# Performance work log

Measured on AMD Instinct MI355X. Metric: run time of the kernel, lower is better.

The kernel has to match this reference:

```python
import jax, jax.numpy as jnp
import numpy as np

EPS = 1e-8
LN_EPS = 1e-5
MA_K = 25


def _moving_avg(x, k):
    # x: [B, L]; replicate-pad by (k-1)//2 on each side, then length-k mean -> [B, L]
    p = (k - 1) // 2
    xp = jnp.concatenate([jnp.repeat(x[:, :1], p, axis=1), x, jnp.repeat(x[:, -1:], p, axis=1)], axis=1)
    cs = jnp.concatenate([jnp.zeros((x.shape[0], 1), x.dtype), jnp.cumsum(xp, axis=1)], axis=1)
    return (cs[:, k:] - cs[:, :-k]) / k


def _acf(xc, den, lag):
    # xc: mean-centered x [B, L]; den: sum(xc^2)+eps [B]
    num = (xc[:, :-lag] * xc[:, lag:]).sum(axis=1)
    return jnp.clip(num / den, -1.0, 1.0)


def _forward(x, ln_w, ln_b, w1, b1, w2, b2):
    B, L = x.shape
    trend = _moving_avg(x, MA_K)
    resid = x - trend

    m = x.mean(axis=1, keepdims=True)
    xc = x - m
    den = (xc * xc).sum(axis=1) + EPS

    acf1 = _acf(xc, den, 1)
    acf2 = _acf(xc, den, 2)

    # spectral entropy + peak psd ratio (single rfft)
    Xf = jnp.fft.rfft(x, axis=1)
    psd = jnp.maximum(Xf.real ** 2 + Xf.imag ** 2, EPS)
    psd_sum = psd.sum(axis=1)
    psd_n = psd / psd_sum[:, None]
    ent = -(psd_n * jnp.log(psd_n + EPS)).sum(axis=1)
    max_ent = jnp.log(jnp.asarray(psd.shape[1], x.dtype) + EPS)
    spent = jnp.clip(ent / (max_ent + EPS), 0.0, 1.0)
    peak_ratio = jnp.clip(psd.max(axis=1) / (psd_sum + EPS), 0.0, 1.0)

    # unit-root phi
    x_t, x_tm1 = x[:, 1:], x[:, :-1]
    phi = jnp.clip((x_t * x_tm1).sum(axis=1) / ((x_tm1 ** 2).sum(axis=1) + EPS), -1.0, 1.0)

    diff = x_t - x_tm1
    diff_var = jnp.var(diff, axis=1)
    trend_strength = jnp.var(trend, axis=1)
    kpss_proxy = jnp.var(jnp.cumsum(resid, axis=1), axis=1) / (jnp.var(x, axis=1) + 1e-8)

    h = max(1, min(10, L // 4))
    lbq = sum(_acf(xc, den, k) ** 2 for k in range(1, h + 1))

    feats = jnp.stack([acf1, acf2, spent, phi, diff_var, trend_strength, kpss_proxy, lbq, peak_ratio], axis=1)

    # LayerNorm over 9 features
    fm = feats.mean(axis=-1, keepdims=True)
    fv = jnp.var(feats, axis=-1, keepdims=True)
    feats_n = (feats - fm) / jnp.sqrt(fv + LN_EPS) * ln_w + ln_b

    # MLP router: 9 -> 64 -> 3 (dropout=0, temperature=1)
    hdd = jax.nn.relu(feats_n @ w1 + b1)
    logits = hdd @ w2 + b2
    weights = jax.nn.softmax(logits, axis=-1)
    return weights, feats_n


def setup_inputs() -> dict:
    key = jax.random.key(0)
    ks = jax.random.split(key, 5)
    B, L, D, H, C = 32768, 1024, 9, 64, 3
    return {
        "x_n_target": jax.random.normal(ks[0], (B, L), dtype=jnp.float32),
        "ln_w": jnp.ones((D,), jnp.float32),
        "ln_b": jnp.zeros((D,), jnp.float32),
        "w1": jax.random.normal(ks[1], (D, H), dtype=jnp.float32) * 0.3,
        "b1": jnp.zeros((H,), jnp.float32),
        "w2": jax.random.normal(ks[2], (H, C), dtype=jnp.float32) * 0.1,
        "b2": jnp.zeros((C,), jnp.float32),
    }


def reference(x_n_target, ln_w, ln_b, w1, b1, w2, b2):
    return _forward(x_n_target, ln_w, ln_b, w1, b1, w2, b2)
```

## Files before the change

kernel.cpp:

```cpp
#include <hip/hip_runtime.h>
#include <math.h>

#define EPSF 1e-8f

typedef float f2v __attribute__((ext_vector_type(2)));

__device__ __forceinline__ float bcf(int x){ return __builtin_bit_cast(float, x); }
__device__ __forceinline__ int   bci(float x){ return __builtin_bit_cast(int, x); }

template<int CTRL, int RM>
__device__ __forceinline__ float dpp0(float v){
  return bcf(__builtin_amdgcn_update_dpp(0, bci(v), CTRL, RM, 0xF, false));
}
__device__ __forceinline__ float rl(float v, int l){
  return bcf(__builtin_amdgcn_readlane(bci(v), l));
}
__device__ __forceinline__ float wave_iscan_add(float v){
  v += dpp0<0x111,0xF>(v);
  v += dpp0<0x112,0xF>(v);
  v += dpp0<0x114,0xF>(v);
  v += dpp0<0x118,0xF>(v);
  v += dpp0<0x142,0xA>(v);
  v += dpp0<0x143,0xC>(v);
  return v;
}
__device__ __forceinline__ float wave_red_add(float v){ return wave_iscan_add(v); }
__device__ __forceinline__ float wave_red_max_pos(float v){
  v = fmaxf(v, dpp0<0x111,0xF>(v));
  v = fmaxf(v, dpp0<0x112,0xF>(v));
  v = fmaxf(v, dpp0<0x114,0xF>(v));
  v = fmaxf(v, dpp0<0x118,0xF>(v));
  v = fmaxf(v, dpp0<0x142,0xA>(v));
  v = fmaxf(v, dpp0<0x143,0xC>(v));
  return v;
}

__device__ __forceinline__ int FL8(int i){ return i ^ ((i >> 3) & 7); }

__device__ __forceinline__ void dft8p(f2v* ar, f2v* ai){
  const float C = 0.70710678118654752f;
  const f2v t0r=ar[0]+ar[4], t0i=ai[0]+ai[4];
  const f2v t1r=ar[0]-ar[4], t1i=ai[0]-ai[4];
  const f2v t2r=ar[2]+ar[6], t2i=ai[2]+ai[6];
  const f2v t3r=ar[2]-ar[6], t3i=ai[2]-ai[6];
  const f2v E0r=t0r+t2r, E0i=t0i+t2i;
  const f2v E1r=t1r+t3i, E1i=t1i-t3r;
  const f2v E2r=t0r-t2r, E2i=t0i-t2i;
  const f2v E3r=t1r-t3i, E3i=t1i+t3r;
  const f2v u0r=ar[1]+ar[5], u0i=ai[1]+ai[5];
  const f2v u1r=ar[1]-ar[5], u1i=ai[1]-ai[5];
  const f2v u2r=ar[3]+ar[7], u2i=ai[3]+ai[7];
  const f2v u3r=ar[3]-ar[7], u3i=ai[3]-ai[7];
  const f2v O0r=u0r+u2r, O0i=u0i+u2i;
  const f2v O1r=u1r+u3i, O1i=u1i-u3r;
  const f2v O2r=u0r-u2r, O2i=u0i-u2i;
  const f2v O3r=u1r-u3i, O3i=u1i+u3r;
  const f2v w1r =  C*(O1r+O1i), w1i = C*(O1i-O1r);
  const f2v w2r =  O2i,         w2i = -O2r;
  const f2v w3r =  C*(O3i-O3r), w3i = -C*(O3r+O3i);
  ar[0]=E0r+O0r; ai[0]=E0i+O0i;
  ar[4]=E0r-O0r; ai[4]=E0i-O0i;
  ar[1]=E1r+w1r; ai[1]=E1i+w1i;
  ar[5]=E1r-w1r; ai[5]=E1i-w1i;
  ar[2]=E2r+w2r; ai[2]=E2i+w2i;
  ar[6]=E2r-w2r; ai[6]=E2i-w2i;
  ar[3]=E3r+w3r; ai[3]=E3i+w3i;
  ar[7]=E3r-w3r; ai[7]=E3i-w3i;
}

__global__ void __launch_bounds__(128, 2)
sr_kernel(const float* __restrict__ x,
          const float* __restrict__ ln_w, const float* __restrict__ ln_b,
          const float* __restrict__ w1, const float* __restrict__ b1,
          const float* __restrict__ w2, const float* __restrict__ b2,
          float* __restrict__ out, int B)
{
  __shared__ __align__(16) float bufr2[2][2048];
  __shared__ __align__(16) float stats2[2][2][40];

  const int tid = threadIdx.x;
  const int t   = tid & 63;
  const int wv  = tid >> 6;
  const int rowbase = blockIdx.x * 4 + wv * 2;
  if (rowbase >= B) return;
  float* buff = bufr2[wv];

#pragma unroll 1
  for (int rr = 0; rr < 2; ++rr) {
    const float* __restrict__ xr = x + (size_t)(rowbase + rr) * 1024;
    float* st = stats2[wv][rr];

    const int c0 = t * 16;
    float vv[28];
    {
      const float4 a0 = *reinterpret_cast<const float4*>(xr + c0);
      const float4 a1 = *reinterpret_cast<const float4*>(xr + c0 + 4);
      const float4 a2 = *reinterpret_cast<const float4*>(xr + c0 + 8);
      const float4 a3 = *reinterpret_cast<const float4*>(xr + c0 + 12);
      vv[0]=a0.x; vv[1]=a0.y; vv[2]=a0.z; vv[3]=a0.w;
      vv[4]=a1.x; vv[5]=a1.y; vv[6]=a1.z; vv[7]=a1.w;
      vv[8]=a2.x; vv[9]=a2.y; vv[10]=a2.z; vv[11]=a2.w;
      vv[12]=a3.x; vv[13]=a3.y; vv[14]=a3.z; vv[15]=a3.w;
      if (t < 63) {
        const float4 n0 = *reinterpret_cast<const float4*>(xr + c0 + 16);
        const float4 n1 = *reinterpret_cast<const float4*>(xr + c0 + 20);
        const float4 n2 = *reinterpret_cast<const float4*>(xr + c0 + 24);
        vv[16]=n0.x; vv[17]=n0.y; vv[18]=n0.z; vv[19]=n0.w;
        vv[20]=n1.x; vv[21]=n1.y; vv[22]=n1.z; vv[23]=n1.w;
        vv[24]=n2.x; vv[25]=n2.y; vv[26]=n2.z; vv[27]=n2.w;
      } else {
#pragma unroll
        for (int j = 16; j < 28; ++j) vv[j] = 0.f;
      }
    }
    float pv[12];
    if (t > 0) {
      const float4 p0 = *reinterpret_cast<const float4*>(xr + c0 - 12);
      const float4 p1 = *reinterpret_cast<const float4*>(xr + c0 - 8);
      const float4 p2 = *reinterpret_cast<const float4*>(xr + c0 - 4);
      pv[0]=p0.x; pv[1]=p0.y; pv[2]=p0.z; pv[3]=p0.w;
      pv[4]=p1.x; pv[5]=p1.y; pv[6]=p1.z; pv[7]=p1.w;
      pv[8]=p2.x; pv[9]=p2.y; pv[10]=p2.z; pv[11]=p2.w;
    } else {
#pragma unroll
      for (int j = 0; j < 12; ++j) pv[j] = 0.f;
    }

#pragma unroll
    for (int j = 0; j < 8; ++j) {
      const int fo = FL8(8*t + j) * 4 + rr;
      buff[fo]     = vv[2*j];
      buff[fo + 2] = vv[2*j + 1];
    }

    {
      float sumsq = 0.f, alt = 0.f;
#pragma unroll
      for (int j = 0; j < 16; ++j) {
        sumsq = fmaf(vv[j], vv[j], sumsq);
        alt += (j & 1) ? -vv[j] : vv[j];
      }
      float r;
      r = wave_red_add(sumsq); if (t == 63) st[0] = r;
      r = wave_red_add(alt);   if (t == 63) st[1] = r;
    }
#pragma unroll
    for (int k = 1; k <= 10; ++k) {
      float acc = 0.f;
#pragma unroll
      for (int j = 0; j < 16; ++j) acc = fmaf(vv[j], vv[j+k], acc);
      float r = wave_red_add(acc);
      if (t == 63) st[1 + k] = r;
    }

    float s[16];
    s[0] = vv[0];
#pragma unroll
    for (int j = 1; j < 16; ++j) s[j] = s[j-1] + vv[j];
    const float cs16 = s[15];
    const float incl = wave_iscan_add(cs16);
    const float excl = incl - cs16;
#pragma unroll
    for (int j = 0; j < 16; ++j) s[j] += excl;
    if (t == 63) st[16] = incl;
    if (t == 0) {
#pragma unroll
      for (int q = 0; q < 10; ++q) st[17 + q] = s[q];
      st[37] = vv[0];
    }
    if (t == 63) {
#pragma unroll
      for (int q = 0; q < 10; ++q) st[27 + q] = s[5 + q];
      st[38] = vv[15];
    }

    float trv[16];
    float str = 0.f, str2 = 0.f;
    {
      float wsum = 0.f;
#pragma unroll
      for (int j = 0; j < 12; ++j) wsum += pv[j];
#pragma unroll
      for (int j = 0; j <= 12; ++j) wsum += vv[j];
#pragma unroll
      for (int jj = 0; jj < 16; ++jj) {
        if (jj > 0) {
          const float addv = vv[jj + 12];
          const float subv = (jj < 13) ? pv[jj - 1] : vv[jj - 13];
          wsum += addv - subv;
        }
        float swc = wsum;
        if (t == 0  && jj < 12) swc += (float)(12 - jj) * vv[0];
        if (t == 63 && jj >= 4) swc += (float)(jj - 3) * vv[15];
        const float tv = swc * 0.04f;
        trv[jj] = tv;
        str += tv;
        str2 = fmaf(tv, tv, str2);
      }
    }
    const float tincl = wave_iscan_add(str);
    if (t == 63) st[12] = tincl;
    { float r = wave_red_add(str2); if (t == 63) st[13] = r; }
    {
      const float texcl = tincl - str;
      float run = texcl, sc = 0.f, sc2 = 0.f;
#pragma unroll
      for (int jj = 0; jj < 16; ++jj) {
        run += trv[jj];
        const float cv = s[jj] - run;
        sc += cv;
        sc2 = fmaf(cv, cv, sc2);
      }
      float r;
      r = wave_red_add(sc);  if (t == 63) st[14] = r;
      r = wave_red_add(sc2); if (t == 63) st[15] = r;
    }
  }

  f2v zr[8], zi[8];
#pragma unroll
  for (int p = 0; p < 8; ++p) {
    const float4 q4 = *reinterpret_cast<const float4*>(&buff[FL8(t + 64*p) * 4]);
    zr[p] = f2v{q4.x, q4.y};
    zi[p] = f2v{q4.z, q4.w};
  }
  dft8p(zr, zi);
  {
    const float a1 = -0.012271846303085130f * (float)t;
    const float c1 = __cosf(a1), s1 = __sinf(a1);
    const float c2=c1*c1-s1*s1, s2=2.f*c1*s1;
    const float c3=c2*c1-s2*s1, s3=s2*c1+c2*s1;
    const float c4=c2*c2-s2*s2, s4=2.f*c2*s2;
    const float c5=c4*c1-s4*s1, s5=s4*c1+c4*s1;
    const float c6=c3*c3-s3*s3, s6=2.f*c3*s3;
    const float c7=c6*c1-s6*s1, s7=s6*c1+c6*s1;
    const float cq[8] = {1.f,c1,c2,c3,c4,c5,c6,c7};
    const float sq[8] = {0.f,s1,s2,s3,s4,s5,s6,s7};
#pragma unroll
    for (int q = 1; q < 8; ++q) {
      const f2v r0 = zr[q]*cq[q] - zi[q]*sq[q];
      zi[q] = zr[q]*sq[q] + zi[q]*cq[q];
      zr[q] = r0;
    }
  }
#pragma unroll
  for (int q = 0; q < 8; ++q) {
    const int fo = FL8(q*64 + t) * 4;
    *reinterpret_cast<f2v*>(&buff[fo])     = zr[q];
    *reinterpret_cast<f2v*>(&buff[fo + 2]) = zi[q];
  }
  const int qq = t >> 3;
  const int dd = t & 7;
  const int qb = qq << 6;
#pragma unroll
  for (int e = 0; e < 8; ++e) {
    const float4 q4 = *reinterpret_cast<const float4*>(&buff[FL8(qb + dd + 8*e) * 4]);
    zr[e] = f2v{q4.x, q4.y};
    zi[e] = f2v{q4.z, q4.w};
  }
  dft8p(zr, zi);
  {
    const float a1 = -0.098174770424681039f * (float)dd;
    const float c1 = __cosf(a1), s1 = __sinf(a1);
    const float c2=c1*c1-s1*s1, s2=2.f*c1*s1;
    const float c3=c2*c1-s2*s1, s3=s2*c1+c2*s1;
    const float c4=c2*c2-s2*s2, s4=2.f*c2*s2;
    const float c5=c4*c1-s4*s1, s5=s4*c1+c4*s1;
    const float c6=c3*c3-s3*s3, s6=2.f*c3*s3;
    const float c7=c6*c1-s6*s1, s7=s6*c1+c6*s1;
    const float cq[8] = {1.f,c1,c2,c3,c4,c5,c6,c7};
    const float sq[8] = {0.f,s1,s2,s3,s4,s5,s6,s7};
#pragma unroll
    for (int q = 1; q < 8; ++q) {
      const f2v r0 = zr[q]*cq[q] - zi[q]*sq[q];
      zi[q] = zr[q]*sq[q] + zi[q]*cq[q];
      zr[q] = r0;
    }
  }
#pragma unroll
  for (int sA = 0; sA < 8; ++sA) {
    const int fo = FL8(qb + sA*8 + dd) * 4;
    *reinterpret_cast<f2v*>(&buff[fo])     = zr[sA];
    *reinterpret_cast<f2v*>(&buff[fo + 2]) = zi[sA];
  }
#pragma unroll
  for (int d = 0; d < 8; ++d) {
    const float4 q4 = *reinterpret_cast<const float4*>(&buff[FL8(qb + dd*8 + d) * 4]);
    zr[d] = f2v{q4.x, q4.y};
    zi[d] = f2v{q4.z, q4.w};
  }
  dft8p(zr, zi);

#pragma unroll
  for (int r = 0; r < 8; ++r) {
    const int fo = FL8(t*8 + r) * 4;
    *reinterpret_cast<f2v*>(&buff[fo])     = zr[r];
    *reinterpret_cast<f2v*>(&buff[fo + 2]) = zi[r];
  }
  const int pl = (t == 0) ? 0 : ((t < 8) ? (8 - t) : (71 - t));
  const bool lane0 = (t == 0);
  const float kb = (float)((dd << 3) + qq);
  const float ab = -0.0061359231515425649f * kb;
  const float wbr = __cosf(ab), wbi = __sinf(ab);
  constexpr float RCr[8] = {1.f, 0.98078528040323044f, 0.92387953251128674f, 0.83146961230254524f,
                            0.70710678118654752f, 0.55557023301960222f, 0.38268343236508977f, 0.19509032201612827f};
  constexpr float RCi[8] = {0.f, -0.19509032201612827f, -0.38268343236508977f, -0.55557023301960222f,
                            -0.70710678118654752f, -0.83146961230254524f, -0.92387953251128674f, -0.98078528040323044f};
  float psA = 0.f, psB = 0.f, pmA = 0.f, pmB = 0.f, plA = 0.f, plB = 0.f;
#pragma unroll
  for (int r = 0; r < 8; ++r) {
    const int rho = lane0 ? ((8 - r) & 7) : (7 - r);
    const float4 q4 = *reinterpret_cast<const float4*>(&buff[FL8(pl*8 + rho) * 4]);
    const f2v zpr = f2v{q4.x, q4.y};
    const f2v zpi = f2v{q4.z, q4.w};
    const f2v Er = 0.5f*(zr[r] + zpr);
    const f2v Ei = 0.5f*(zi[r] - zpi);
    const f2v Or = 0.5f*(zi[r] + zpi);
    const f2v Oi = -0.5f*(zr[r] - zpr);
    const float wr = wbr*RCr[r] - wbi*RCi[r];
    const float wi = wbr*RCi[r] + wbi*RCr[r];
    const f2v Xr = Er + wr*Or - wi*Oi;
    const f2v Xi = Ei + wr*Oi + wi*Or;
    const f2v pp = Xr*Xr + Xi*Xi;
    const float pa = fmaxf(pp.x, EPSF);
    const float pb = fmaxf(pp.y, EPSF);
    psA += pa; psB += pb;
    pmA = fmaxf(pmA, pa); pmB = fmaxf(pmB, pb);
    plA += pa * __logf(pa);
    plB += pb * __logf(pb);
  }
  float PSUM2[2], PMAX2[2], PLOG2[2];
  PSUM2[0] = rl(wave_red_add(psA), 63);
  PSUM2[1] = rl(wave_red_add(psB), 63);
  PMAX2[0] = rl(wave_red_max_pos(pmA), 63);
  PMAX2[1] = rl(wave_red_max_pos(pmB), 63);
  PLOG2[0] = rl(wave_red_add(plA), 63);
  PLOG2[1] = rl(wave_red_add(plB), 63);

#pragma unroll 1
  for (int rr = 0; rr < 2; ++rr) {
    const float* st = stats2[wv][rr];
    const int row = rowbase + rr;
    const float PSUM = PSUM2[rr], PMAX = PMAX2[rr], PLOG = PLOG2[rr];

    const float SUMSQ = st[0];
    const float ALT   = st[1];
    const float STR   = st[12];
    const float STR2  = st[13];
    const float SC    = st[14];
    const float SC2   = st[15];
    const float SUMX  = st[16];
    const float x0    = st[37];
    const float xl    = st[38];

    const float p512b = fmaxf(ALT * ALT, EPSF);
    const float Sr    = PSUM + p512b;
    const float invS  = 1.f / Sr;
    const float PLr   = PLOG + p512b * __logf(p512b);
    const float ent   = __logf(Sr) - PLr * invS;
    const float PMX   = fmaxf(PMAX, p512b);

    const float m = SUMX * (1.f / 1024.f);
    const float den = SUMSQ - 1024.f * m * m + EPSF;
    const float invden = 1.f / den;
    float acf1 = 0.f, acf2 = 0.f, lbq = 0.f, R1v = 0.f;
#pragma unroll
    for (int k = 1; k <= 10; ++k) {
      const float Rkv = st[1 + k];
      const float Slo = st[16 + k];
      const float Shi = st[37 - k];
      const float num = Rkv - m * (Shi + (SUMX - Slo)) + (float)(1024 - k) * m * m;
      const float a = fminf(fmaxf(num * invden, -1.f), 1.f);
      if (k == 1) { acf1 = a; R1v = Rkv; }
      else if (k == 2) acf2 = a;
      lbq += a * a;
    }
    const float spent = fminf(fmaxf(ent / (__logf(513.f + EPSF) + EPSF), 0.f), 1.f);
    const float peak  = fminf(fmaxf(PMX / (Sr + EPSF), 0.f), 1.f);
    const float phi = fminf(fmaxf(R1v / ((SUMSQ - xl * xl) + EPSF), -1.f), 1.f);
    const float invn = 1.f / 1023.f;
    const float sum_d2 = 2.f * SUMSQ - x0 * x0 - xl * xl - 2.f * R1v;
    const float md = (xl - x0) * invn;
    const float diff_var = sum_d2 * invn - md * md;
    const float tstr = STR2 * (1.f / 1024.f) - (STR * (1.f / 1024.f)) * (STR * (1.f / 1024.f));
    const float varx = SUMSQ * (1.f / 1024.f) - m * m;
    const float mc = SC * (1.f / 1024.f);
    const float kpss = (SC2 * (1.f / 1024.f) - mc * mc) / (varx + 1e-8f);

    float f[9] = {acf1, acf2, spent, phi, diff_var, tstr, kpss, lbq, peak};
    float fm = 0.f;
#pragma unroll
    for (int d = 0; d < 9; ++d) fm += f[d];
    fm *= (1.f / 9.f);
    float fv = 0.f;
#pragma unroll
    for (int d = 0; d < 9; ++d) { const float tt = f[d] - fm; fv = fmaf(tt, tt, fv); }
    fv *= (1.f / 9.f);
    const float inl = 1.f / sqrtf(fv + 1e-5f);
    float fn[9];
#pragma unroll
    for (int d = 0; d < 9; ++d) fn[d] = (f[d] - fm) * inl * ln_w[d] + ln_b[d];

    float h = b1[t];
#pragma unroll
    for (int d = 0; d < 9; ++d) h = fmaf(fn[d], w1[d * 64 + t], h);
    h = fmaxf(h, 0.f);
    float l0 = h * w2[t * 3 + 0];
    float l1 = h * w2[t * 3 + 1];
    float l2 = h * w2[t * 3 + 2];
    l0 = wave_red_add(l0);
    l1 = wave_red_add(l1);
    l2 = wave_red_add(l2);
    const float L0 = rl(l0, 63) + b2[0];
    const float L1 = rl(l1, 63) + b2[1];
    const float L2 = rl(l2, 63) + b2[2];
    if (t == 0) {
      const float mx = fmaxf(L0, fmaxf(L1, L2));
      const float e0 = __expf(L0 - mx), e1 = __expf(L1 - mx), e2 = __expf(L2 - mx);
      const float is = 1.f / (e0 + e1 + e2);
      float* o = out + (size_t)row * 3;
      o[0] = e0 * is; o[1] = e1 * is; o[2] = e2 * is;
      float* fo = out + (size_t)B * 3 + (size_t)row * 9;
      fo[0] = fn[0]; fo[1] = fn[1]; fo[2] = fn[2]; fo[3] = fn[3]; fo[4] = fn[4];
      fo[5] = fn[5]; fo[6] = fn[6]; fo[7] = fn[7]; fo[8] = fn[8];
    }
  }
}

extern "C" void kernel_launch(void* const* d_in, const int* in_sizes, int n_in,
                              void* d_out, int out_size, void* d_ws, size_t ws_size,
                              hipStream_t stream) {
  (void)n_in; (void)out_size; (void)d_ws; (void)ws_size;
  const float* x    = (const float*)d_in[0];
  const float* ln_w = (const float*)d_in[1];
  const float* ln_b = (const float*)d_in[2];
  const float* w1   = (const float*)d_in[3];
  const float* b1   = (const float*)d_in[4];
  const float* w2   = (const float*)d_in[5];
  const float* b2   = (const float*)d_in[6];
  float* out = (float*)d_out;
  const int B = in_sizes[0] / 1024;
  sr_kernel<<<(B + 3) / 4, 128, 0, stream>>>(x, ln_w, ln_b, w1, b1, w2, b2, out, B);
}
```

Baseline: 82.90 us.

## Process two rows jointly with packed float2 math reading halos from LDS

The per-row loop is split. A first phase only loads each row, writes the interleaved LDS buffer and computes the prefix scan. The ACF lags, moving-average trend and cumulative-residual statistics are then computed for both rows at once using float2 vectors (packed FP32 ops) read back from the LDS buffer, replacing the redundant global halo loads. This halves the VALU instruction count for those stats and removes overlapping global reads, at the cost of extra LDS reads and reading st[37]/st[38] from shared memory without an explicit barrier (same wave, so likely safe).

Result: slower. 86.85 us (+4.8%).

```diff
diff --git a/kernel.cpp b/kernel.cpp
--- a/kernel.cpp
+++ b/kernel.cpp
@@ -84,14 +84,15 @@
   const int rowbase = blockIdx.x * 4 + wv * 2;
   if (rowbase >= B) return;
   float* buff = bufr2[wv];
-
-#pragma unroll 1
-  for (int rr = 0; rr < 2; ++rr) {
+  float* stA  = stats2[wv][0];
+  float* stB  = stats2[wv][1];
+
+  float exclA, exclB;
+  auto phase1 = [&](int rr, float& excl_out) {
     const float* __restrict__ xr = x + (size_t)(rowbase + rr) * 1024;
-    float* st = stats2[wv][rr];
-
+    float* st = rr ? stB : stA;
     const int c0 = t * 16;
-    float vv[28];
+    float vv[16];
     {
       const float4 a0 = *reinterpret_cast<const float4*>(xr + c0);
       const float4 a1 = *reinterpret_cast<const float4*>(xr + c0 + 4);
@@ -101,58 +102,13 @@
       vv[4]=a1.x; vv[5]=a1.y; vv[6]=a1.z; vv[7]=a1.w;
       vv[8]=a2.x; vv[9]=a2.y; vv[10]=a2.z; vv[11]=a2.w;
       vv[12]=a3.x; vv[13]=a3.y; vv[14]=a3.z; vv[15]=a3.w;
-      if (t < 63) {
-        const float4 n0 = *reinterpret_cast<const float4*>(xr + c0 + 16);
-        const float4 n1 = *reinterpret_cast<const float4*>(xr + c0 + 20);
-        const float4 n2 = *reinterpret_cast<const float4*>(xr + c0 + 24);
-        vv[16]=n0.x; vv[17]=n0.y; vv[18]=n0.z; vv[19]=n0.w;
-        vv[20]=n1.x; vv[21]=n1.y; vv[22]=n1.z; vv[23]=n1.w;
-        vv[24]=n2.x; vv[25]=n2.y; vv[26]=n2.z; vv[27]=n2.w;
-      } else {
-#pragma unroll
-        for (int j = 16; j < 28; ++j) vv[j] = 0.f;
-      }
-    }
-    float pv[12];
-    if (t > 0) {
-      const float4 p0 = *reinterpret_cast<const float4*>(xr + c0 - 12);
-      const float4 p1 = *reinterpret_cast<const float4*>(xr + c0 - 8);
-      const float4 p2 = *reinterpret_cast<const float4*>(xr + c0 - 4);
-      pv[0]=p0.x; pv[1]=p0.y; pv[2]=p0.z; pv[3]=p0.w;
-      pv[4]=p1.x; pv[5]=p1.y; pv[6]=p1.z; pv[7]=p1.w;
-      pv[8]=p2.x; pv[9]=p2.y; pv[10]=p2.z; pv[11]=p2.w;
-    } else {
-#pragma unroll
-      for (int j = 0; j < 12; ++j) pv[j] = 0.f;
-    }
-
+    }
 #pragma unroll
     for (int j = 0; j < 8; ++j) {
       const int fo = FL8(8*t + j) * 4 + rr;
       buff[fo]     = vv[2*j];
       buff[fo + 2] = vv[2*j + 1];
     }
-
-    {
-      float sumsq = 0.f, alt = 0.f;
-#pragma unroll
-      for (int j = 0; j < 16; ++j) {
-        sumsq = fmaf(vv[j], vv[j], sumsq);
-        alt += (j & 1) ? -vv[j] : vv[j];
-      }
-      float r;
-      r = wave_red_add(sumsq); if (t == 63) st[0] = r;
-      r = wave_red_add(alt);   if (t == 63) st[1] = r;
-    }
-#pragma unroll
-    for (int k = 1; k <= 10; ++k) {
-      float acc = 0.f;
-#pragma unroll
-      for (int j = 0; j < 16; ++j) acc = fmaf(vv[j], vv[j+k], acc);
-      float r = wave_red_add(acc);
-      if (t == 63) st[1 + k] = r;
-    }
-
     float s[16];
     s[0] = vv[0];
 #pragma unroll
@@ -160,6 +116,7 @@
     const float cs16 = s[15];
     const float incl = wave_iscan_add(cs16);
     const float excl = incl - cs16;
+    excl_out = excl;
 #pragma unroll
     for (int j = 0; j < 16; ++j) s[j] += excl;
     if (t == 63) st[16] = incl;
@@ -173,48 +130,115 @@
       for (int q = 0; q < 10; ++q) st[27 + q] = s[5 + q];
       st[38] = vv[15];
     }
-
-    float trv[16];
-    float str = 0.f, str2 = 0.f;
-    {
-      float wsum = 0.f;
-#pragma unroll
-      for (int j = 0; j < 12; ++j) wsum += pv[j];
-#pragma unroll
-      for (int j = 0; j <= 12; ++j) wsum += vv[j];
-#pragma unroll
-      for (int jj = 0; jj < 16; ++jj) {
-        if (jj > 0) {
-          const float addv = vv[jj + 12];
-          const float subv = (jj < 13) ? pv[jj - 1] : vv[jj - 13];
-          wsum += addv - subv;
-        }
-        float swc = wsum;
-        if (t == 0  && jj < 12) swc += (float)(12 - jj) * vv[0];
-        if (t == 63 && jj >= 4) swc += (float)(jj - 3) * vv[15];
-        const float tv = swc * 0.04f;
-        trv[jj] = tv;
-        str += tv;
-        str2 = fmaf(tv, tv, str2);
+  };
+  phase1(0, exclA);
+  phase1(1, exclB);
+
+  f2v xv[28];
+#pragma unroll
+  for (int u = 0; u < 8; ++u) {
+    const float4 q4 = *reinterpret_cast<const float4*>(&buff[FL8(8*t + u) * 4]);
+    xv[2*u]   = f2v{q4.x, q4.y};
+    xv[2*u+1] = f2v{q4.z, q4.w};
+  }
+  if (t < 63) {
+#pragma unroll
+    for (int u = 0; u < 6; ++u) {
+      const float4 q4 = *reinterpret_cast<const float4*>(&buff[FL8(8*t + 8 + u) * 4]);
+      xv[16+2*u]   = f2v{q4.x, q4.y};
+      xv[16+2*u+1] = f2v{q4.z, q4.w};
+    }
+  } else {
+#pragma unroll
+    for (int j = 16; j < 28; ++j) xv[j] = f2v{0.f, 0.f};
+  }
+  f2v pxv[12];
+  if (t > 0) {
+#pragma unroll
+    for (int u = 0; u < 6; ++u) {
+      const float4 q4 = *reinterpret_cast<const float4*>(&buff[FL8(8*t - 6 + u) * 4]);
+      pxv[2*u]   = f2v{q4.x, q4.y};
+      pxv[2*u+1] = f2v{q4.z, q4.w};
+    }
+  } else {
+#pragma unroll
+    for (int j = 0; j < 12; ++j) pxv[j] = f2v{0.f, 0.f};
+  }
+
+  {
+    f2v sumsq2 = {0.f,0.f}, alt2 = {0.f,0.f};
+#pragma unroll
+    for (int j = 0; j < 16; ++j) {
+      sumsq2 += xv[j] * xv[j];
+      alt2 += (j & 1) ? -xv[j] : xv[j];
+    }
+    float r;
+    r = wave_red_add(sumsq2.x); if (t == 63) stA[0] = r;
+    r = wave_red_add(sumsq2.y); if (t == 63) stB[0] = r;
+    r = wave_red_add(alt2.x);   if (t == 63) stA[1] = r;
+    r = wave_red_add(alt2.y);   if (t == 63) stB[1] = r;
+  }
+#pragma unroll
+  for (int k = 1; k <= 10; ++k) {
+    f2v acc = {0.f,0.f};
+#pragma unroll
+    for (int j = 0; j < 16; ++j) acc += xv[j] * xv[j+k];
+    float r;
+    r = wave_red_add(acc.x); if (t == 63) stA[1 + k] = r;
+    r = wave_red_add(acc.y); if (t == 63) stB[1 + k] = r;
+  }
+
+  const f2v x0p = f2v{stA[37], stB[37]};
+  const f2v xlp = f2v{stA[38], stB[38]};
+  f2v trv2[16];
+  f2v strv = {0.f,0.f}, strsq = {0.f,0.f};
+  {
+    f2v wsum = {0.f,0.f};
+#pragma unroll
+    for (int j = 0; j < 12; ++j) wsum += pxv[j];
+#pragma unroll
+    for (int j = 0; j <= 12; ++j) wsum += xv[j];
+#pragma unroll
+    for (int jj = 0; jj < 16; ++jj) {
+      if (jj > 0) {
+        const f2v addv = xv[jj + 12];
+        const f2v subv = (jj < 13) ? pxv[jj - 1] : xv[jj - 13];
+        wsum += addv - subv;
       }
-    }
-    const float tincl = wave_iscan_add(str);
-    if (t == 63) st[12] = tincl;
-    { float r = wave_red_add(str2); if (t == 63) st[13] = r; }
-    {
-      const float texcl = tincl - str;
-      float run = texcl, sc = 0.f, sc2 = 0.f;
-#pragma unroll
-      for (int jj = 0; jj < 16; ++jj) {
-        run += trv[jj];
-        const float cv = s[jj] - run;
-        sc += cv;
-        sc2 = fmaf(cv, cv, sc2);
-      }
-      float r;
-      r = wave_red_add(sc);  if (t == 63) st[14] = r;
-      r = wave_red_add(sc2); if (t == 63) st[15] = r;
-    }
+      f2v swc = wsum;
+      if (t == 0  && jj < 12) swc += (float)(12 - jj) * x0p;
+      if (t == 63 && jj >= 4) swc += (float)(jj - 3) * xlp;
+      const f2v tv = swc * 0.04f;
+      trv2[jj] = tv;
+      strv += tv;
+      strsq += tv * tv;
+    }
+  }
+  const float tinclA = wave_iscan_add(strv.x);
+  const float tinclB = wave_iscan_add(strv.y);
+  if (t == 63) { stA[12] = tinclA; stB[12] = tinclB; }
+  {
+    float r;
+    r = wave_red_add(strsq.x); if (t == 63) stA[13] = r;
+    r = wave_red_add(strsq.y); if (t == 63) stB[13] = r;
+  }
+  {
+    f2v run  = f2v{tinclA, tinclB} - strv;
+    f2v pref = f2v{exclA, exclB};
+    f2v sc = {0.f,0.f}, scs = {0.f,0.f};
+#pragma unroll
+    for (int jj = 0; jj < 16; ++jj) {
+      pref += xv[jj];
+      run  += trv2[jj];
+      const f2v c = pref - run;
+      sc  += c;
+      scs += c * c;
+    }
+    float r;
+    r = wave_red_add(sc.x);  if (t == 63) stA[14] = r;
+    r = wave_red_add(sc.y);  if (t == 63) stB[14] = r;
+    r = wave_red_add(scs.x); if (t == 63) stA[15] = r;
+    r = wave_red_add(scs.y); if (t == 63) stB[15] = r;
   }
 
   f2v zr[8], zi[8];
```
